# Performance work log

Measured on AMD Instinct MI355X. Metric: run time of the kernel, lower is better.

## Reference

```python
import jax, jax.numpy as jnp
import numpy as np

EMBED = 384
HEADS = 6
HEAD_SIZE = EMBED // HEADS
EPS = 1e-5


def _layernorm(x, g, b):
    mu = jnp.mean(x, axis=-1, keepdims=True)
    var = jnp.mean(jnp.square(x - mu), axis=-1, keepdims=True)
    return (x - mu) * jax.lax.rsqrt(var + EPS) * g + b


def setup_inputs() -> dict:
    key = jax.random.key(0)
    ks = jax.random.split(key, 16)
    B, T = 64, 256
    s_in = 1.0 / np.sqrt(EMBED)
    return {
        "x": jax.random.normal(ks[0], (B, T, EMBED), dtype=jnp.float32),
        # per-head q/k/v projections, stacked over heads: [H, C, D]
        "Wq": jax.random.normal(ks[1], (HEADS, EMBED, HEAD_SIZE), dtype=jnp.float32) * s_in,
        "bq": jnp.zeros((HEADS, HEAD_SIZE), dtype=jnp.float32),
        "Wk": jax.random.normal(ks[2], (HEADS, EMBED, HEAD_SIZE), dtype=jnp.float32) * s_in,
        "bk": jnp.zeros((HEADS, HEAD_SIZE), dtype=jnp.float32),
        "Wv": jax.random.normal(ks[3], (HEADS, EMBED, HEAD_SIZE), dtype=jnp.float32) * s_in,
        "bv": jnp.zeros((HEADS, HEAD_SIZE), dtype=jnp.float32),
        "Wp": jax.random.normal(ks[4], (EMBED, EMBED), dtype=jnp.float32) * s_in,
        "bp": jnp.zeros((EMBED,), dtype=jnp.float32),
        "W1": jax.random.normal(ks[5], (EMBED, EMBED), dtype=jnp.float32) * s_in,
        "b1": jnp.zeros((EMBED,), dtype=jnp.float32),
        "W2": jax.random.normal(ks[6], (EMBED, EMBED), dtype=jnp.float32) * s_in,
        "b2": jnp.zeros((EMBED,), dtype=jnp.float32),
        "ln1_g": jnp.ones((EMBED,), dtype=jnp.float32),
        "ln1_b": jnp.zeros((EMBED,), dtype=jnp.float32),
        "ln2_g": jnp.ones((EMBED,), dtype=jnp.float32),
        "ln2_b": jnp.zeros((EMBED,), dtype=jnp.float32),
    }


def reference(x, Wq, bq, Wk, bk, Wv, bv, Wp, bp, W1, b1, W2, b2,
              ln1_g, ln1_b, ln2_g, ln2_b):
    B, T, C = x.shape
    h = _layernorm(x, ln1_g, ln1_b)
    # batched per-head projections: [B,H,T,D]
    q = jnp.einsum('btc,hcd->bhtd', h, Wq) + bq[None, :, None, :]
    k = jnp.einsum('btc,hcd->bhtd', h, Wk) + bk[None, :, None, :]
    v = jnp.einsum('btc,hcd->bhtd', h, Wv) + bv[None, :, None, :]
    # NOTE: original scales by embed_size**0.5 (C=384), not head_size.
    wei = jnp.einsum('bhtd,bhsd->bhts', q, k) / jnp.sqrt(jnp.float32(C))
    causal = jnp.tril(jnp.ones((T, T), dtype=bool))
    wei = jnp.where(causal[None, None], wei, -jnp.inf)
    wei = jax.nn.softmax(wei, axis=-1)  # dropout = identity in eval
    attn = jnp.einsum('bhts,bhsd->bhtd', wei, v)  # [B,H,T,D]
    # concat heads in head order -> [B,T,C]
    attn = attn.transpose(0, 2, 1, 3).reshape(B, T, C)
    x = x + attn @ Wp + bp
    h2 = _layernorm(x, ln2_g, ln2_b)
    ff = jax.nn.relu(h2 @ W1 + b1) @ W2 + b2
    return x + ff
```

## Files before the change

kernel.cpp:

```cpp
#include <hip/hip_runtime.h>

typedef _Float16 f16;
typedef _Float16 half8 __attribute__((ext_vector_type(8)));
typedef _Float16 half4v __attribute__((ext_vector_type(4)));
typedef float floatx4 __attribute__((ext_vector_type(4)));

#define B_ 64
#define T_ 256
#define C_ 384
#define H_ 6
#define D_ 64
#define NROWS (B_*T_)

typedef __attribute__((address_space(3))) void lds_void_t;
typedef const __attribute__((address_space(1))) void gvoid_t;

__device__ __forceinline__ void g2lds16(const void* g, void* l) {
  __builtin_amdgcn_global_load_lds((gvoid_t*)g, (lds_void_t*)l, 16, 0, 0);
}

__global__ __launch_bounds__(256) void prep_kernel(
    const float* __restrict__ Wq, const float* __restrict__ Wk, const float* __restrict__ Wv,
    const float* __restrict__ bq, const float* __restrict__ bk, const float* __restrict__ bv,
    const float* __restrict__ Wp, const float* __restrict__ W1, const float* __restrict__ W2,
    f16* __restrict__ Wqkv_t, f16* __restrict__ Wp_t, f16* __restrict__ W1_t, f16* __restrict__ W2_t,
    float* __restrict__ bqkv)
{
  const int bid = blockIdx.x;
  const int tid = threadIdx.x;
  if (bid == 216) {
    for (int i = tid; i < 1152; i += 256) {
      float v;
      if (i < 384)      v = bq[i];
      else if (i < 768) v = bk[i - 384];
      else              v = bv[i - 768];
      bqkv[i] = v;
    }
    return;
  }
  __shared__ __align__(16) float tile[64*68];
  const float* src; int srcStride; f16* dst;
  if (bid < 108) {
    int mat = bid / 36, rem = bid - mat*36;
    int h = rem / 6, kt = rem - h*6;
    const float* W = (mat == 0) ? Wq : (mat == 1) ? Wk : Wv;
    src = W + (size_t)(h*384 + kt*64)*64;
    srcStride = 64;
    dst = Wqkv_t + (size_t)(mat*384 + h*64)*384 + kt*64;
  } else {
    int b2 = bid - 108;
    int mat = b2 / 36, rem = b2 - mat*36;
    int kt = rem / 6, ct = rem - kt*6;
    const float* W = (mat == 0) ? Wp : (mat == 1) ? W1 : W2;
    src = W + (size_t)(kt*64)*384 + ct*64;
    srcStride = 384;
    f16* O = (mat == 0) ? Wp_t : (mat == 1) ? W1_t : W2_t;
    dst = O + (size_t)(ct*64)*384 + kt*64;
  }
#pragma unroll
  for (int i = 0; i < 4; i++) {
    int idx = i*256 + tid;
    int r = idx >> 4, c4 = idx & 15;
    float4 v = *(const float4*)(src + (size_t)r*srcStride + c4*4);
    *(float4*)(&tile[r*68 + c4*4]) = v;
  }
  __syncthreads();
#pragma unroll
  for (int i = 0; i < 4; i++) {
    int idx = i*256 + tid;
    int d = idx >> 4, k4 = idx & 15;
    half4v o;
#pragma unroll
    for (int j = 0; j < 4; j++) o[j] = (f16)tile[(k4*4 + j)*68 + d];
    *(half4v*)(dst + (size_t)d*384 + k4*4) = o;
  }
}

__global__ __launch_bounds__(256) void ln_kernel(const float* __restrict__ x,
    const float* __restrict__ gamma, const float* __restrict__ beta, f16* __restrict__ out)
{
  int row = blockIdx.x * 4 + (threadIdx.x >> 6);
  int lane = threadIdx.x & 63;
  const float* xr = x + (size_t)row * 384;
  float v[6]; float s = 0.f;
#pragma unroll
  for (int j = 0; j < 6; j++) { v[j] = xr[lane + 64*j]; s += v[j]; }
#pragma unroll
  for (int m = 1; m < 64; m <<= 1) s += __shfl_xor(s, m);
  float mu = s * (1.f/384.f);
  float var = 0.f;
#pragma unroll
  for (int j = 0; j < 6; j++) { float d = v[j]-mu; var += d*d; }
#pragma unroll
  for (int m = 1; m < 64; m <<= 1) var += __shfl_xor(var, m);
  float rs = rsqrtf(var * (1.f/384.f) + 1e-5f);
  f16* orow = out + (size_t)row*384;
#pragma unroll
  for (int j = 0; j < 6; j++) {
    int col = lane + 64*j;
    orow[col] = (f16)((v[j]-mu)*rs*gamma[col] + beta[col]);
  }
}

template<int MODE>
__global__ __launch_bounds__(256) void gemm_kernel(
    const f16* __restrict__ A, const f16* __restrict__ Bt,
    const float* __restrict__ bias, const float* __restrict__ res,
    void* __restrict__ outp, int ldo)
{
  __shared__ __align__(16) f16 As[128*32];
  __shared__ __align__(16) f16 Bs[128*32];
  const int tid = threadIdx.x;
  const int lane = tid & 63, w = tid >> 6;
  const int wm = w >> 1, wn = w & 1;
  const int q = lane >> 4, c15 = lane & 15;
  const long row0 = (long)blockIdx.x * 128;
  const long col0 = (long)blockIdx.y * 128;
  floatx4 acc[4][4] = {};

  const int c0 = tid,        r0c = c0 >> 2, p0 = c0 & 3, g0 = p0 ^ ((r0c >> 1) & 3);
  const int c1 = 256 + tid,  r1c = c1 >> 2, p1 = c1 & 3, g1 = p1 ^ ((r1c >> 1) & 3);
  const f16* Arow0 = A  + (row0 + r0c)*384 + g0*8;
  const f16* Arow1 = A  + (row0 + r1c)*384 + g1*8;
  const f16* Brow0 = Bt + (col0 + r0c)*384 + g0*8;
  const f16* Brow1 = Bt + (col0 + r1c)*384 + g1*8;
  f16* Adst0 = As + (w*64)*8;
  f16* Adst1 = As + (256 + w*64)*8;
  f16* Bdst0 = Bs + (w*64)*8;
  f16* Bdst1 = Bs + (256 + w*64)*8;

  for (int k0 = 0; k0 < 384; k0 += 32) {
    g2lds16(Arow0 + k0, Adst0);
    g2lds16(Arow1 + k0, Adst1);
    g2lds16(Brow0 + k0, Bdst0);
    g2lds16(Brow1 + k0, Bdst1);
    __syncthreads();
    half8 af[4], bf[4];
#pragma unroll
    for (int mi = 0; mi < 4; mi++) {
      int r = wm*64 + mi*16 + c15;
      int ph = q ^ ((r >> 1) & 3);
      af[mi] = *(const half8*)(As + r*32 + ph*8);
    }
#pragma unroll
    for (int ni = 0; ni < 4; ni++) {
      int r = wn*64 + ni*16 + c15;
      int ph = q ^ ((r >> 1) & 3);
      bf[ni] = *(const half8*)(Bs + r*32 + ph*8);
    }
#pragma unroll
    for (int mi = 0; mi < 4; mi++)
#pragma unroll
      for (int ni = 0; ni < 4; ni++)
        acc[mi][ni] = __builtin_amdgcn_mfma_f32_16x16x32_f16(af[mi], bf[ni], acc[mi][ni], 0, 0, 0);
    __syncthreads();
  }

#pragma unroll
  for (int ni = 0; ni < 4; ni++) {
    long col = col0 + wn*64 + ni*16 + c15;
    float bv = bias[col];
#pragma unroll
    for (int mi = 0; mi < 4; mi++) {
      long rowb = row0 + wm*64 + mi*16 + q*4;
#pragma unroll
      for (int r = 0; r < 4; r++) {
        float vo = acc[mi][ni][r] + bv;
        if (MODE == 1) vo = vo > 0.f ? vo : 0.f;
        long o = (rowb + r) * (long)ldo + col;
        if (MODE == 2) {
          ((float*)outp)[o] = vo + res[o];
        } else {
          ((f16*)outp)[o] = (f16)vo;
        }
      }
    }
  }
}

__global__ __launch_bounds__(256, 3) void attn_kernel(const f16* __restrict__ qkv,
                                                      f16* __restrict__ attn_out)
{
  __shared__ __align__(16) char kvbuf[32768];
  __shared__ __align__(16) f16 Pbuf[4][16*128];
  f16* Ks = (f16*)kvbuf;
  unsigned int* vTw = (unsigned int*)kvbuf;
  f16* vT = (f16*)kvbuf;

  const int tid = threadIdx.x;
  const int bid = blockIdx.x;
  const int bh = bid >> 2, qt = bid & 3;
  const int b = bh / 6, h = bh - b*6;
  const f16* qp = qkv + (size_t)b*256*1152 + h*64;
  const f16* kp = qp + 384;
  const f16* vp = qp + 768;
  const int lane = tid & 63, w = tid >> 6;
  const int q = lane >> 4, c15 = lane & 15;

  {
    const int iters = (qt + 1) * 2;
    const int pcbase = w*64 + lane;
    for (int i = 0; i < iters; i++) {
      int pc = i*256 + pcbase;
      int rc = pc >> 3, p = pc & 7;
      int c = p ^ (rc & 7);
      g2lds16(kp + (size_t)rc*1152 + c*8, (char*)kvbuf + (size_t)(i*256 + w*64)*16);
    }
  }
  __syncthreads();

  const int nmax = qt*4 + w;
  const int trow0 = qt*64 + w*16;
  const f16* qrow = qp + (size_t)(trow0 + c15)*1152 + q*8;
  half8 aq0 = *(const half8*)(qrow);
  half8 aq1 = *(const half8*)(qrow + 32);

  floatx4 sacc[16];
#pragma unroll
  for (int ni = 0; ni < 16; ni++) {
    if (ni <= nmax) {
      int s = ni*16 + c15;
      const f16* kr = Ks + s*64;
      int p0 = q ^ (s & 7);
      half8 b0 = *(const half8*)(kr + p0*8);
      half8 b1 = *(const half8*)(kr + (p0 ^ 4)*8);
      floatx4 a = {0.f, 0.f, 0.f, 0.f};
      a = __builtin_amdgcn_mfma_f32_16x16x32_f16(aq0, b0, a, 0, 0, 0);
      a = __builtin_amdgcn_mfma_f32_16x16x32_f16(aq1, b1, a, 0, 0, 0);
      sacc[ni] = a;
    }
  }

  const float scale = 0.051031036307982884f;
  float mx[4] = {-1e30f, -1e30f, -1e30f, -1e30f};
#pragma unroll
  for (int ni = 0; ni < 16; ni++) {
    if (ni < nmax) {
#pragma unroll
      for (int r = 0; r < 4; r++) { float v = sacc[ni][r]*scale; sacc[ni][r] = v; mx[r] = fmaxf(mx[r], v); }
    } else if (ni == nmax) {
#pragma unroll
      for (int r = 0; r < 4; r++) {
        float v = sacc[ni][r]*scale;
        v = (c15 <= q*4 + r) ? v : -1e30f;
        sacc[ni][r] = v; mx[r] = fmaxf(mx[r], v);
      }
    }
  }
#pragma unroll
  for (int r = 0; r < 4; r++) {
    mx[r] = fmaxf(mx[r], __shfl_xor(mx[r], 1));
    mx[r] = fmaxf(mx[r], __shfl_xor(mx[r], 2));
    mx[r] = fmaxf(mx[r], __shfl_xor(mx[r], 4));
    mx[r] = fmaxf(mx[r], __shfl_xor(mx[r], 8));
  }
  float l[4] = {0.f, 0.f, 0.f, 0.f};
#pragma unroll
  for (int ni = 0; ni < 16; ni++) {
    if (ni <= nmax) {
#pragma unroll
      for (int r = 0; r < 4; r++) { float p = __expf(sacc[ni][r] - mx[r]); sacc[ni][r] = p; l[r] += p; }
    }
  }
#pragma unroll
  for (int r = 0; r < 4; r++) {
    l[r] += __shfl_xor(l[r], 1);
    l[r] += __shfl_xor(l[r], 2);
    l[r] += __shfl_xor(l[r], 4);
    l[r] += __shfl_xor(l[r], 8);
  }
  __syncthreads();

  {
    const int iters = qt + 1;
    for (int i = 0; i < iters; i++) {
      int idx = i*256 + tid;
      int sp = idx >> 3, part = idx & 7;
      const f16* v0 = vp + (size_t)(2*sp)*1152 + part*8;
      half8 va = *(const half8*)(v0);
      half8 vb = *(const half8*)(v0 + 1152);
      int csp = sp >> 2, spw = sp & 3;
#pragma unroll
      for (int j = 0; j < 8; j++) {
        int d = part*8 + j;
        int swz = (d & 15) ^ (d >> 3);
        int p = csp ^ swz;
        union { struct { f16 lo, hi; } s; unsigned int u; } pk;
        pk.s.lo = va[j]; pk.s.hi = vb[j];
        vTw[d*128 + p*4 + spw] = pk.u;
      }
    }
  }
  __syncthreads();

  f16* Pw = &Pbuf[w][0];
  floatx4 oacc[4] = {};
  const int kend_w = (nmax + 1) * 16;
#pragma unroll
  for (int ch = 0; ch < 2; ch++) {
    if (ch*128 < kend_w) {
#pragma unroll
      for (int nl = 0; nl < 8; nl++) {
        int ni = ch*8 + nl;
        if (ni <= nmax) {
#pragma unroll
          for (int r = 0; r < 4; r++) {
            int row = q*4 + r;
            int colp = nl*16 + c15;
            int php = (colp >> 3) ^ row;
            Pw[row*128 + php*8 + (colp & 7)] = (f16)sacc[ni][r];
          }
        } else if (ni == nmax + 1) {
#pragma unroll
          for (int r = 0; r < 4; r++) {
            int row = q*4 + r;
            int colp = nl*16 + c15;
            int php = (colp >> 3) ^ row;
            Pw[row*128 + php*8 + (colp & 7)] = (f16)0.f;
          }
        }
      }
#pragma unroll
      for (int kc = 0; kc < 4; kc++) {
        if (ch*128 + kc*32 < kend_w) {
          int pc = (kc*4 + q) ^ c15;
          half8 ap = *(const half8*)(Pw + c15*128 + pc*8);
          int sc = ch*16 + kc*4 + q;
#pragma unroll
          for (int nt = 0; nt < 4; nt++) {
            int d = nt*16 + c15;
            int swz = (d & 15) ^ (d >> 3);
            half8 bv = *(const half8*)(vT + d*256 + ((sc ^ swz))*8);
            oacc[nt] = __builtin_amdgcn_mfma_f32_16x16x32_f16(ap, bv, oacc[nt], 0, 0, 0);
          }
        }
      }
    }
  }

#pragma unroll
  for (int nt = 0; nt < 4; nt++) {
#pragma unroll
    for (int r = 0; r < 4; r++) {
      int t = trow0 + q*4 + r;
      int d = nt*16 + c15;
      attn_out[(size_t)(b*256 + t)*384 + h*64 + d] = (f16)(oacc[nt][r] / l[r]);
    }
  }
}

extern "C" void kernel_launch(void* const* d_in, const int* in_sizes, int n_in,
                              void* d_out, int out_size, void* d_ws, size_t ws_size,
                              hipStream_t stream) {
  const float* x   = (const float*)d_in[0];
  const float* Wq  = (const float*)d_in[1];
  const float* bq  = (const float*)d_in[2];
  const float* Wk  = (const float*)d_in[3];
  const float* bk  = (const float*)d_in[4];
  const float* Wv  = (const float*)d_in[5];
  const float* bv  = (const float*)d_in[6];
  const float* Wp  = (const float*)d_in[7];
  const float* bp  = (const float*)d_in[8];
  const float* W1  = (const float*)d_in[9];
  const float* b1  = (const float*)d_in[10];
  const float* W2  = (const float*)d_in[11];
  const float* b2  = (const float*)d_in[12];
  const float* g1  = (const float*)d_in[13];
  const float* be1 = (const float*)d_in[14];
  const float* g2  = (const float*)d_in[15];
  const float* be2 = (const float*)d_in[16];

  char* ws = (char*)d_ws;
  size_t off = 0;
  auto alloc = [&](size_t bytes) -> void* {
    void* p = ws + off;
    off += (bytes + 255) & ~(size_t)255;
    return p;
  };
  f16*   Wqkv_t = (f16*)  alloc(1152*384*sizeof(f16));
  f16*   Wp_t   = (f16*)  alloc(384*384*sizeof(f16));
  f16*   W1_t   = (f16*)  alloc(384*384*sizeof(f16));
  f16*   W2_t   = (f16*)  alloc(384*384*sizeof(f16));
  float* bqkv   = (float*)alloc(1152*sizeof(float));
  f16*   h      = (f16*)  alloc((size_t)NROWS*384*sizeof(f16));
  f16*   qkv    = (f16*)  alloc((size_t)NROWS*1152*sizeof(f16));
  f16*   attnb  = (f16*)  alloc((size_t)NROWS*384*sizeof(f16));
  float* x2     = (float*)alloc((size_t)NROWS*384*sizeof(float));
  f16*   h2     = (f16*)  alloc((size_t)NROWS*384*sizeof(f16));
  f16*   mid    = (f16*)  alloc((size_t)NROWS*384*sizeof(f16));

  prep_kernel<<<217, 256, 0, stream>>>(Wq, Wk, Wv, bq, bk, bv, Wp, W1, W2,
                                       Wqkv_t, Wp_t, W1_t, W2_t, bqkv);
  ln_kernel<<<NROWS/4, 256, 0, stream>>>(x, g1, be1, h);
  gemm_kernel<0><<<dim3(128, 9), 256, 0, stream>>>(h, Wqkv_t, bqkv, nullptr, qkv, 1152);
  attn_kernel<<<B_*H_*4, 256, 0, stream>>>(qkv, attnb);
  gemm_kernel<2><<<dim3(128, 3), 256, 0, stream>>>(attnb, Wp_t, bp, x, x2, 384);
  ln_kernel<<<NROWS/4, 256, 0, stream>>>(x2, g2, be2, h2);
  gemm_kernel<1><<<dim3(128, 3), 256, 0, stream>>>(h2, W1_t, b1, nullptr, mid, 384);
  gemm_kernel<2><<<dim3(128, 3), 256, 0, stream>>>(mid, W2_t, b2, x2, (float*)d_out, 384);
}
```

Baseline: 215.1 us.

## Merge weight prep with first layernorm; double GEMM k-step per barrier

Folds the first layernorm into the weight-conversion kernel as extra blocks, which removes one kernel launch and lets the two independent jobs run concurrently. The GEMM now loads two 32-wide k slices into separate LDS buffers before each barrier pair, so each K=384 loop takes half as many barriers. This doubles LDS per block, which may lower occupancy. Loads are still not overlapped with compute.

Result: faster. 204.6 us, median of 2 (-4.9%).

```diff
diff --git a/kernel.cpp b/kernel.cpp
--- a/kernel.cpp
+++ b/kernel.cpp
@@ -19,15 +19,41 @@
   __builtin_amdgcn_global_load_lds((gvoid_t*)g, (lds_void_t*)l, 16, 0, 0);
 }
 
-__global__ __launch_bounds__(256) void prep_kernel(
+__global__ __launch_bounds__(256) void prep_ln_kernel(
     const float* __restrict__ Wq, const float* __restrict__ Wk, const float* __restrict__ Wv,
     const float* __restrict__ bq, const float* __restrict__ bk, const float* __restrict__ bv,
     const float* __restrict__ Wp, const float* __restrict__ W1, const float* __restrict__ W2,
     f16* __restrict__ Wqkv_t, f16* __restrict__ Wp_t, f16* __restrict__ W1_t, f16* __restrict__ W2_t,
-    float* __restrict__ bqkv)
+    float* __restrict__ bqkv,
+    const float* __restrict__ x, const float* __restrict__ gamma, const float* __restrict__ beta,
+    f16* __restrict__ hout)
 {
   const int bid = blockIdx.x;
   const int tid = threadIdx.x;
+  if (bid >= 217) {
+    int row = (bid - 217) * 4 + (tid >> 6);
+    int lane = tid & 63;
+    const float* xr = x + (size_t)row * 384;
+    float v[6]; float s = 0.f;
+#pragma unroll
+    for (int j = 0; j < 6; j++) { v[j] = xr[lane + 64*j]; s += v[j]; }
+#pragma unroll
+    for (int m = 1; m < 64; m <<= 1) s += __shfl_xor(s, m);
+    float mu = s * (1.f/384.f);
+    float var = 0.f;
+#pragma unroll
+    for (int j = 0; j < 6; j++) { float d = v[j]-mu; var += d*d; }
+#pragma unroll
+    for (int m = 1; m < 64; m <<= 1) var += __shfl_xor(var, m);
+    float rs = rsqrtf(var * (1.f/384.f) + 1e-5f);
+    f16* orow = hout + (size_t)row*384;
+#pragma unroll
+    for (int j = 0; j < 6; j++) {
+      int col = lane + 64*j;
+      orow[col] = (f16)((v[j]-mu)*rs*gamma[col] + beta[col]);
+    }
+    return;
+  }
   if (bid == 216) {
     for (int i = tid; i < 1152; i += 256) {
       float v;
@@ -108,8 +134,8 @@
     const float* __restrict__ bias, const float* __restrict__ res,
     void* __restrict__ outp, int ldo)
 {
-  __shared__ __align__(16) f16 As[128*32];
-  __shared__ __align__(16) f16 Bs[128*32];
+  __shared__ __align__(16) f16 As[2][128*32];
+  __shared__ __align__(16) f16 Bs[2][128*32];
   const int tid = threadIdx.x;
   const int lane = tid & 63, w = tid >> 6;
   const int wm = w >> 1, wn = w & 1;
@@ -124,35 +150,39 @@
   const f16* Arow1 = A  + (row0 + r1c)*384 + g1*8;
   const f16* Brow0 = Bt + (col0 + r0c)*384 + g0*8;
   const f16* Brow1 = Bt + (col0 + r1c)*384 + g1*8;
-  f16* Adst0 = As + (w*64)*8;
-  f16* Adst1 = As + (256 + w*64)*8;
-  f16* Bdst0 = Bs + (w*64)*8;
-  f16* Bdst1 = Bs + (256 + w*64)*8;
-
-  for (int k0 = 0; k0 < 384; k0 += 32) {
-    g2lds16(Arow0 + k0, Adst0);
-    g2lds16(Arow1 + k0, Adst1);
-    g2lds16(Brow0 + k0, Bdst0);
-    g2lds16(Brow1 + k0, Bdst1);
+  const int dof0 = (w*64)*8, dof1 = (256 + w*64)*8;
+
+  for (int k0 = 0; k0 < 384; k0 += 64) {
+#pragma unroll
+    for (int hf = 0; hf < 2; hf++) {
+      int kk = k0 + hf*32;
+      g2lds16(Arow0 + kk, &As[hf][dof0]);
+      g2lds16(Arow1 + kk, &As[hf][dof1]);
+      g2lds16(Brow0 + kk, &Bs[hf][dof0]);
+      g2lds16(Brow1 + kk, &Bs[hf][dof1]);
+    }
     __syncthreads();
-    half8 af[4], bf[4];
-#pragma unroll
-    for (int mi = 0; mi < 4; mi++) {
-      int r = wm*64 + mi*16 + c15;
-      int ph = q ^ ((r >> 1) & 3);
-      af[mi] = *(const half8*)(As + r*32 + ph*8);
-    }
-#pragma unroll
-    for (int ni = 0; ni < 4; ni++) {
-      int r = wn*64 + ni*16 + c15;
-      int ph = q ^ ((r >> 1) & 3);
-      bf[ni] = *(const half8*)(Bs + r*32 + ph*8);
-    }
-#pragma unroll
-    for (int mi = 0; mi < 4; mi++)
-#pragma unroll
-      for (int ni = 0; ni < 4; ni++)
-        acc[mi][ni] = __builtin_amdgcn_mfma_f32_16x16x32_f16(af[mi], bf[ni], acc[mi][ni], 0, 0, 0);
+#pragma unroll
+    for (int hf = 0; hf < 2; hf++) {
+      half8 af[4], bf[4];
+#pragma unroll
+      for (int mi = 0; mi < 4; mi++) {
+        int r = wm*64 + mi*16 + c15;
+        int ph = q ^ ((r >> 1) & 3);
+        af[mi] = *(const half8*)(&As[hf][r*32 + ph*8]);
+      }
+#pragma unroll
+      for (int ni = 0; ni < 4; ni++) {
+        int r = wn*64 + ni*16 + c15;
+        int ph = q ^ ((r >> 1) & 3);
+        bf[ni] = *(const half8*)(&Bs[hf][r*32 + ph*8]);
+      }
+#pragma unroll
+      for (int mi = 0; mi < 4; mi++)
+#pragma unroll
+        for (int ni = 0; ni < 4; ni++)
+          acc[mi][ni] = __builtin_amdgcn_mfma_f32_16x16x32_f16(af[mi], bf[ni], acc[mi][ni], 0, 0, 0);
+    }
     __syncthreads();
   }
 
@@ -389,9 +419,9 @@
   f16*   h2     = (f16*)  alloc((size_t)NROWS*384*sizeof(f16));
   f16*   mid    = (f16*)  alloc((size_t)NROWS*384*sizeof(f16));
 
-  prep_kernel<<<217, 256, 0, stream>>>(Wq, Wk, Wv, bq, bk, bv, Wp, W1, W2,
-                                       Wqkv_t, Wp_t, W1_t, W2_t, bqkv);
-  ln_kernel<<<NROWS/4, 256, 0, stream>>>(x, g1, be1, h);
+  prep_ln_kernel<<<217 + NROWS/4, 256, 0, stream>>>(Wq, Wk, Wv, bq, bk, bv, Wp, W1, W2,
+                                                    Wqkv_t, Wp_t, W1_t, W2_t, bqkv,
+                                                    x, g1, be1, h);
   gemm_kernel<0><<<dim3(128, 9), 256, 0, stream>>>(h, Wqkv_t, bqkv, nullptr, qkv, 1152);
   attn_kernel<<<B_*H_*4, 256, 0, stream>>>(qkv, attnb);
   gemm_kernel<2><<<dim3(128, 3), 256, 0, stream>>>(attnb, Wp_t, bp, x, x2, 384);
```
